# Optimization experiments

Hardware: AMD Instinct MI355X
Metric: run time of the kernel (lower is better)

## Reference

```python
import jax, jax.numpy as jnp
import numpy as np

V, E, H, B, T, O = 32000, 512, 1024, 128, 512, 1
PAD_IDX = 0


def setup_inputs() -> dict:
    key = jax.random.key(0)
    ks = jax.random.split(key, 20)
    std = 1.0 / np.sqrt(H)
    u = lambda k, shape: jax.random.uniform(k, shape, jnp.float32, -std, std)
    inp = {
        "x": jax.random.randint(ks[0], (B, T), 0, V),
        "lengths": jax.random.randint(ks[1], (B,), 1, T + 1),
        "emb": jax.random.normal(ks[2], (V, E), jnp.float32),
        "W_ii": u(ks[3], (H, E)), "W_hi": u(ks[4], (H, H)), "b_i": u(ks[5], (H,)),
        "W_if": u(ks[6], (H, E)), "W_hf": u(ks[7], (H, H)), "b_f": u(ks[8], (H,)),
        "W_ig": u(ks[9], (H, E)), "W_hg": u(ks[10], (H, H)), "b_g": u(ks[11], (H,)),
        "W_io": u(ks[12], (H, E)), "W_ho": u(ks[13], (H, H)), "b_o": u(ks[14], (H,)),
        "fc_w": u(ks[15], (O, H)), "fc_b": u(ks[16], (O,)),
    }
    return inp


def reference(x, lengths, emb, W_ii, W_hi, b_i, W_if, W_hf, b_f,
              W_ig, W_hg, b_g, W_io, W_ho, b_o, fc_w, fc_b):
    # padding_idx row is frozen at zero (matches nn.Embedding(padding_idx=...))
    emb = emb.at[PAD_IDX].set(0.0)
    xe = emb[x]  # [B, T, E]

    # stack the 4 gate projections (same math, one GEMM): gate order i, f, g, o
    Wi = jnp.concatenate([W_ii, W_if, W_ig, W_io], axis=0)  # [4H, E]
    Wh = jnp.concatenate([W_hi, W_hf, W_hg, W_ho], axis=0)  # [4H, H]
    b = jnp.concatenate([b_i, b_f, b_g, b_o], axis=0)       # [4H]

    # precompute all input contributions in one big GEMM: [B, T, 4H]
    xp = jnp.einsum('bte,ge->btg', xe, Wi) + b
    xp_t = jnp.transpose(xp, (1, 0, 2))  # [T, B, 4H]

    h0 = jnp.zeros((B, H), jnp.float32)
    c0 = jnp.zeros((B, H), jnp.float32)
    out0 = jnp.zeros((B, H), jnp.float32)
    ts = jnp.arange(T)

    def step(carry, inputs):
        h, c, out = carry
        xpt, t = inputs
        z = xpt + h @ Wh.T  # [B, 4H]
        i_t = jax.nn.sigmoid(z[:, 0 * H:1 * H])
        f_t = jax.nn.sigmoid(z[:, 1 * H:2 * H])
        g_t = jnp.tanh(z[:, 2 * H:3 * H])
        o_t = jax.nn.sigmoid(z[:, 3 * H:4 * H])
        c = f_t * c + i_t * g_t
        h = o_t * jnp.tanh(c)
        mask = (lengths == t + 1)[:, None]  # [B, 1]
        out = jnp.where(mask, h, out)
        return (h, c, out), None

    (_, _, outputs), _ = jax.lax.scan(step, (h0, c0, out0), (xp_t, ts))
    return outputs @ fc_w.T + fc_b  # [B, O]
```

## Files before the change

kernel.cpp:

```cpp
#include <hip/hip_runtime.h>
#include <math.h>

#define Bsz 128
#define Tsz 512
#define Esz 512
#define Hsz 1024
#define G4H 4096
#define Vsz 32000
#define NB  64
#define BH  (Bsz * Hsz)
#define XPS 68

typedef __attribute__((ext_vector_type(8))) short short8;
typedef __attribute__((ext_vector_type(4))) short short4v;
typedef __attribute__((ext_vector_type(8))) __bf16 bf16x8;
typedef __attribute__((ext_vector_type(4))) float f32x4;
typedef __attribute__((ext_vector_type(4))) unsigned int uint4v;

__device__ inline unsigned short f2bf(float f) {
    unsigned u = __float_as_uint(f);
    u += 0x7fffu + ((u >> 16) & 1u);
    return (unsigned short)(u >> 16);
}
__device__ inline float bf2f(unsigned short s) {
    return __uint_as_float(((unsigned)s) << 16);
}
__device__ inline f32x4 mfma16(short8 a, short8 b, f32x4 c) {
    return __builtin_amdgcn_mfma_f32_16x16x32_bf16(
        __builtin_bit_cast(bf16x8, a), __builtin_bit_cast(bf16x8, b), c, 0, 0, 0);
}

#define GLD16P(dst, p)  asm volatile("global_load_dwordx4 %0, %1, off"         : "=&v"(dst) : "v"(p))
#define GLD16C(dst, p)  asm volatile("global_load_dwordx4 %0, %1, off sc0 sc1" : "=&v"(dst) : "v"(p))

#define WAITVM(n)                                                          \
    do { asm volatile("s_waitcnt vmcnt(" #n ")" ::: "memory");             \
         __builtin_amdgcn_sched_barrier(0); } while (0)

__device__ inline unsigned ld_flag(const unsigned* p) {
    unsigned r;
    asm volatile("global_load_dword %0, %1, off sc0 sc1\n\ts_waitcnt vmcnt(0)"
                 : "=&v"(r) : "v"(p) : "memory");
    return r;
}
__device__ inline void st_flag(unsigned* p, unsigned v) {
    asm volatile("global_store_dword %0, %1, off sc0 sc1" :: "v"(p), "v"(v) : "memory");
}

__global__ void k_prep_emb(const float* __restrict__ emb, unsigned short* __restrict__ dst) {
    size_t i = (size_t)blockIdx.x * 256 + threadIdx.x;
    if (i < (size_t)Vsz * Esz) dst[i] = f2bf(i < Esz ? 0.f : emb[i]);
}

__global__ void k_prep_w(const float* __restrict__ wi, const float* __restrict__ wf,
                         const float* __restrict__ wg, const float* __restrict__ wo,
                         int ncols, unsigned short* __restrict__ dst) {
    size_t i = (size_t)blockIdx.x * 256 + threadIdx.x;
    size_t per = (size_t)Hsz * ncols;
    if (i < 4 * per) {
        int g = (int)(i / per);
        size_t rem = i - (size_t)g * per;
        const float* src = g == 0 ? wi : g == 1 ? wf : g == 2 ? wg : wo;
        dst[i] = f2bf(src[rem]);
    }
}

__global__ void k_prep_misc(const float* __restrict__ bi, const float* __restrict__ bff,
                            const float* __restrict__ bg, const float* __restrict__ bo,
                            float* __restrict__ b4, unsigned short* __restrict__ ghbuf,
                            float* __restrict__ cbuf, float* __restrict__ outh,
                            unsigned* __restrict__ flags) {
    int i = blockIdx.x * 256 + threadIdx.x;
    if (i < G4H) {
        const float* src = i < Hsz ? bi : i < 2 * Hsz ? bff : i < 3 * Hsz ? bg : bo;
        b4[i] = src[i & (Hsz - 1)];
    }
    if (i < 2 * BH) ghbuf[i] = 0;
    if (i < BH) { cbuf[i] = 0.f; outh[i] = 0.f; }
    if (i < NB * 32) flags[i] = 0u;
}

__global__ __launch_bounds__(256, 2) void xp_gemm(
    const unsigned short* __restrict__ emb16, const unsigned short* __restrict__ Wi16,
    const float* __restrict__ b4, const int* __restrict__ x,
    unsigned short* __restrict__ xp, int t_base)
{
    const int tp = blockIdx.x;
    const int n0 = blockIdx.y * 128;
    const int tid = threadIdx.x;
    const int w = tid >> 6, l = tid & 63;
    const int wm = w >> 1, wn = w & 1;
    const int lr = l & 15, lk = l >> 4;

    const unsigned short* arow[4];
    #pragma unroll
    for (int mt = 0; mt < 4; ++mt) {
        int b = wm * 64 + mt * 16 + lr;
        int xv = x[b * Tsz + t_base + tp];
        arow[mt] = emb16 + (size_t)xv * Esz + lk * 8;
    }
    const unsigned short* brow[4];
    #pragma unroll
    for (int nt = 0; nt < 4; ++nt) {
        int n = n0 + wn * 64 + nt * 16 + lr;
        brow[nt] = Wi16 + (size_t)n * Esz + lk * 8;
    }
    f32x4 acc[4][4] = {};
    #pragma unroll 2
    for (int k0 = 0; k0 < Esz; k0 += 32) {
        short8 av[4], bv[4];
        #pragma unroll
        for (int mt = 0; mt < 4; ++mt) av[mt] = *(const short8*)(arow[mt] + k0);
        #pragma unroll
        for (int nt = 0; nt < 4; ++nt) bv[nt] = *(const short8*)(brow[nt] + k0);
        #pragma unroll
        for (int mt = 0; mt < 4; ++mt)
            #pragma unroll
            for (int nt = 0; nt < 4; ++nt)
                acc[mt][nt] = mfma16(av[mt], bv[nt], acc[mt][nt]);
    }
    #pragma unroll
    for (int nt = 0; nt < 4; ++nt) {
        int n = n0 + wn * 64 + nt * 16 + lr;
        float bias = b4[n];
        int g = n >> 10, j = n & 1023;
        int bk = j >> 4, jj = j & 15;
        #pragma unroll
        for (int mt = 0; mt < 4; ++mt) {
            #pragma unroll
            for (int r = 0; r < 4; ++r) {
                int b = wm * 64 + mt * 16 + lk * 4 + r;
                xp[((size_t)tp * NB + bk) * (Bsz * 64) + b * 64 + jj * 4 + g] =
                    f2bf(acc[mt][nt][r] + bias);
            }
        }
    }
}

__global__ __launch_bounds__(512, 1) void lstm_steps(
    const unsigned short* __restrict__ Wh16,
    const unsigned short* __restrict__ xp,
    const int* __restrict__ lengths,
    unsigned short* __restrict__ ghbuf,
    float* __restrict__ cbuf,
    float* __restrict__ outh,
    unsigned* __restrict__ flags,
    int t0, int nsteps)
{
    __shared__ unsigned short Whs[64][1032];
    __shared__ unsigned short xps[Bsz * XPS];
    __shared__ unsigned short hls[Bsz * 16];
    const int tid = threadIdx.x;
    const int blk = blockIdx.x;
    const int j0 = blk * 16;

    for (int idx = tid; idx < 64 * 128; idx += 512) {
        int n = idx >> 7, gq = idx & 127;
        int grow = (n >> 4) * Hsz + j0 + (n & 15);
        *(short8*)&Whs[n][gq << 3] =
            *(const short8*)(Wh16 + (size_t)grow * Hsz + gq * 8);
    }

    const int w = tid >> 6, l = tid & 63, lr = l & 15, lk = l >> 4;

    int lenr[4];
    float creg[4];
    #pragma unroll
    for (int r = 0; r < 4; ++r) {
        int b = 16 * w + 4 * lk + r;
        lenr[r] = lengths[b];
        creg[r] = cbuf[(size_t)b * Hsz + j0 + lr];
    }

    {
        const short8* sp = (const short8*)(xp + (size_t)blk * (Bsz * 64));
        int xb = tid >> 2, xq = tid & 3;
        *(short8*)&xps[xb * XPS + xq * 16]     = sp[tid * 2];
        *(short8*)&xps[xb * XPS + xq * 16 + 8] = sp[tid * 2 + 1];
    }
    __syncthreads();

    const int hb_off = (lk >> 1) * 2048 + (lk & 1) * 8 + (16 * w + lr) * 16;

#define ISSUE_CHUNK(buf, kc_) do {                                         \
        GLD16C(buf[0], hb + (kc_) * 16384 + 0);                            \
        GLD16C(buf[1], hb + (kc_) * 16384 + 4096);                         \
        GLD16C(buf[2], hb + (kc_) * 16384 + 8192);                         \
        GLD16C(buf[3], hb + (kc_) * 16384 + 12288);                        \
    } while (0)

#define CONSUME(buf, kc_) do {                                             \
        _Pragma("unroll")                                                  \
        for (int ks_ = 0; ks_ < 4; ++ks_) {                                \
            short8 a_ = __builtin_bit_cast(short8, buf[ks_]);              \
            const int go_ = ((kc_) * 16 + ks_ * 4 + lk) << 3;              \
            _Pragma("unroll")                                              \
            for (int nt_ = 0; nt_ < 4; ++nt_) {                            \
                short8 bv_ = *(const short8*)&Whs[nt_ * 16 + lr][go_];     \
                acc[nt_] = mfma16(a_, bv_, acc[nt_]);                      \
            }                                                              \
        }                                                                  \
    } while (0)

    for (int s = 0; s < nsteps; ++s) {
        const int t = t0 + s;
        const unsigned short* hb = ghbuf + (size_t)(t & 1) * BH + hb_off;
        int sn = (s + 1 < nsteps) ? s + 1 : s;
        const unsigned short* xpn = xp + ((size_t)sn * NB + blk) * (Bsz * 64) + tid * 16;

        f32x4 acc[4] = {};
        uint4v A[4], Bb[4], xr0, xr1;
        ISSUE_CHUNK(A, 0);  ISSUE_CHUNK(Bb, 1);
        WAITVM(4);  CONSUME(A, 0);   ISSUE_CHUNK(A, 2);
        WAITVM(4);  CONSUME(Bb, 1);  ISSUE_CHUNK(Bb, 3);
        WAITVM(4);  CONSUME(A, 2);   ISSUE_CHUNK(A, 4);
        WAITVM(4);  CONSUME(Bb, 3);  ISSUE_CHUNK(Bb, 5);
        WAITVM(4);  CONSUME(A, 4);   ISSUE_CHUNK(A, 6);
        WAITVM(4);  CONSUME(Bb, 5);  ISSUE_CHUNK(Bb, 7);
        GLD16P(xr0, xpn); GLD16P(xr1, xpn + 8);
        WAITVM(6);  CONSUME(A, 6);
        WAITVM(2);  CONSUME(Bb, 7);

        #pragma unroll
        for (int r = 0; r < 4; ++r) {
            int b = 16 * w + 4 * lk + r;
            short4v xg4 = *(const short4v*)&xps[b * XPS + lr * 4];
            float zi = acc[0][r] + bf2f((unsigned short)xg4[0]);
            float zf = acc[1][r] + bf2f((unsigned short)xg4[1]);
            float zg = acc[2][r] + bf2f((unsigned short)xg4[2]);
            float zo = acc[3][r] + bf2f((unsigned short)xg4[3]);
            float it = 1.f / (1.f + __expf(-zi));
            float ft = 1.f / (1.f + __expf(-zf));
            float gt = tanhf(zg);
            float ot = 1.f / (1.f + __expf(-zo));
            float c = ft * creg[r] + it * gt;
            creg[r] = c;
            float h = ot * tanhf(c);
            if (lenr[r] == t + 1) outh[(size_t)b * Hsz + j0 + lr] = h;
            hls[b * 16 + lr] = f2bf(h);
        }
        __syncthreads();

        unsigned short* ghn = ghbuf + (size_t)((t + 1) & 1) * BH;
        if (tid < 256) {
            short8 hv8 = *(const short8*)&hls[tid * 8];
            unsigned short* hd = ghn + (size_t)blk * 2048 + tid * 8;
            asm volatile("global_store_dwordx4 %0, %1, off sc0 sc1"
                         :: "v"(hd), "v"(__builtin_bit_cast(uint4v, hv8)) : "memory");
        }

        WAITVM(0);
        {
            int xb = tid >> 2, xq = tid & 3;
            *(short8*)&xps[xb * XPS + xq * 16]     = __builtin_bit_cast(short8, xr0);
            *(short8*)&xps[xb * XPS + xq * 16 + 8] = __builtin_bit_cast(short8, xr1);
        }
        __syncthreads();

        if (tid == 0) st_flag(&flags[blk * 32], (unsigned)(t + 1));
        {
            const unsigned* fp = &flags[(tid & 63) * 32];
            while (ld_flag(fp) < (unsigned)(t + 1)) __builtin_amdgcn_s_sleep(1);
        }
        __syncthreads();
        __builtin_amdgcn_sched_barrier(0);
    }

    #pragma unroll
    for (int r = 0; r < 4; ++r) {
        int b = 16 * w + 4 * lk + r;
        cbuf[(size_t)b * Hsz + j0 + lr] = creg[r];
    }
#undef ISSUE_CHUNK
#undef CONSUME
}

__global__ __launch_bounds__(64) void k_fc(const float* __restrict__ outh,
                                           const float* __restrict__ fc_w,
                                           const float* __restrict__ fc_b,
                                           float* __restrict__ out) {
    int b = blockIdx.x, l = threadIdx.x;
    float s = 0.f;
    for (int k = l; k < Hsz; k += 64) s += outh[(size_t)b * Hsz + k] * fc_w[k];
    #pragma unroll
    for (int o = 32; o > 0; o >>= 1) s += __shfl_down(s, o);
    if (l == 0) out[b] = s + fc_b[0];
}

extern "C" void kernel_launch(void* const* d_in, const int* in_sizes, int n_in,
                              void* d_out, int out_size, void* d_ws, size_t ws_size,
                              hipStream_t stream) {
    const int* x       = (const int*)d_in[0];
    const int* lengths = (const int*)d_in[1];
    const float* emb   = (const float*)d_in[2];
    const float* W_ii  = (const float*)d_in[3];
    const float* W_hi  = (const float*)d_in[4];
    const float* b_i   = (const float*)d_in[5];
    const float* W_if  = (const float*)d_in[6];
    const float* W_hf  = (const float*)d_in[7];
    const float* b_f   = (const float*)d_in[8];
    const float* W_ig  = (const float*)d_in[9];
    const float* W_hg  = (const float*)d_in[10];
    const float* b_g   = (const float*)d_in[11];
    const float* W_io  = (const float*)d_in[12];
    const float* W_ho  = (const float*)d_in[13];
    const float* b_o   = (const float*)d_in[14];
    const float* fc_w  = (const float*)d_in[15];
    const float* fc_b  = (const float*)d_in[16];
    float* out = (float*)d_out;

    char* ws = (char*)d_ws;
    size_t off = 0;
    auto take = [&](size_t bytes) { size_t o = off; off += (bytes + 255) & ~(size_t)255; return o; };
    unsigned* flags       = (unsigned*)(ws + take((size_t)NB * 128));
    unsigned short* ghbuf = (unsigned short*)(ws + take((size_t)2 * BH * 2));
    float* cbuf           = (float*)(ws + take((size_t)BH * 4));
    float* outh           = (float*)(ws + take((size_t)BH * 4));
    float* b4             = (float*)(ws + take((size_t)G4H * 4));
    unsigned short* Wi16  = (unsigned short*)(ws + take((size_t)G4H * Esz * 2));
    unsigned short* Wh16  = (unsigned short*)(ws + take((size_t)G4H * Hsz * 2));
    unsigned short* emb16 = (unsigned short*)(ws + take((size_t)Vsz * Esz * 2));
    size_t fixed = off;

    int TC = 128;
    while (TC > 1 && fixed + (size_t)TC * Bsz * G4H * 2 > ws_size) TC >>= 1;
    unsigned short* xp = (unsigned short*)(ws + take((size_t)TC * Bsz * G4H * 2));

    k_prep_emb<<<(Vsz * Esz + 255) / 256, 256, 0, stream>>>(emb, emb16);
    k_prep_w<<<(4 * Hsz * Esz + 255) / 256, 256, 0, stream>>>(W_ii, W_if, W_ig, W_io, Esz, Wi16);
    k_prep_w<<<(4 * Hsz * Hsz + 255) / 256, 256, 0, stream>>>(W_hi, W_hf, W_hg, W_ho, Hsz, Wh16);
    k_prep_misc<<<(2 * BH + 255) / 256, 256, 0, stream>>>(b_i, b_f, b_g, b_o, b4, ghbuf, cbuf, outh, flags);

    for (int c = 0; c < Tsz / TC; ++c) {
        dim3 g(TC, 32);
        xp_gemm<<<g, 256, 0, stream>>>(emb16, Wi16, b4, x, xp, c * TC);
        lstm_steps<<<NB, 512, 0, stream>>>(Wh16, xp, lengths, ghbuf, cbuf, outh, flags, c * TC, TC);
    }
    k_fc<<<Bsz, 64, 0, stream>>>(outh, fc_w, fc_b, out);
}
```

Baseline: 4.809 ms.

## Switch recurrent step to 32x32x16 MFMA with 4 waves per block

Rewrites the persistent LSTM step kernel so each block uses 256 threads (4 waves) instead of 512. Each wave now computes a 32-batch by 64-gate tile with 32x32x16 bf16 MFMAs in place of 16x16x32 ones. The h loads are deepened to four chunks of eight 16-byte loads in flight, and a lane shuffle realigns the gate outputs before the elementwise update. The aim is fewer MFMA issues and fewer LDS reads of the weights per step. In exchange each wave does twice the per-lane elementwise work, uses more registers, and the block has fewer waves to hide the latency of the per-step grid barrier.

```diff
diff --git a/kernel.cpp b/kernel.cpp
--- a/kernel.cpp
+++ b/kernel.cpp
@@ -14,6 +14,7 @@
 typedef __attribute__((ext_vector_type(8))) short short8;
 typedef __attribute__((ext_vector_type(4))) short short4v;
 typedef __attribute__((ext_vector_type(8))) __bf16 bf16x8;
+typedef __attribute__((ext_vector_type(16))) float f32x16;
 typedef __attribute__((ext_vector_type(4))) float f32x4;
 typedef __attribute__((ext_vector_type(4))) unsigned int uint4v;
 
@@ -27,6 +28,10 @@
 }
 __device__ inline f32x4 mfma16(short8 a, short8 b, f32x4 c) {
     return __builtin_amdgcn_mfma_f32_16x16x32_bf16(
+        __builtin_bit_cast(bf16x8, a), __builtin_bit_cast(bf16x8, b), c, 0, 0, 0);
+}
+__device__ inline f32x16 mfma32(short8 a, short8 b, f32x16 c) {
+    return __builtin_amdgcn_mfma_f32_32x32x16_bf16(
         __builtin_bit_cast(bf16x8, a), __builtin_bit_cast(bf16x8, b), c, 0, 0, 0);
 }
 
@@ -137,7 +142,7 @@
     }
 }
 
-__global__ __launch_bounds__(512, 1) void lstm_steps(
+__global__ __launch_bounds__(256, 1) void lstm_steps(
     const unsigned short* __restrict__ Wh16,
     const unsigned short* __restrict__ xp,
     const int* __restrict__ lengths,
@@ -154,51 +159,62 @@
     const int blk = blockIdx.x;
     const int j0 = blk * 16;
 
-    for (int idx = tid; idx < 64 * 128; idx += 512) {
+    for (int idx = tid; idx < 64 * 128; idx += 256) {
         int n = idx >> 7, gq = idx & 127;
         int grow = (n >> 4) * Hsz + j0 + (n & 15);
         *(short8*)&Whs[n][gq << 3] =
             *(const short8*)(Wh16 + (size_t)grow * Hsz + gq * 8);
     }
 
-    const int w = tid >> 6, l = tid & 63, lr = l & 15, lk = l >> 4;
-
-    int lenr[4];
-    float creg[4];
-    #pragma unroll
-    for (int r = 0; r < 4; ++r) {
-        int b = 16 * w + 4 * lk + r;
-        lenr[r] = lengths[b];
-        creg[r] = cbuf[(size_t)b * Hsz + j0 + lr];
+    const int w = tid >> 6, l = tid & 63;
+    const int c31 = l & 31, jj = l & 15;
+    const int hi = (l >> 5) & 1;
+    const int hib = (l >> 4) & 1;
+    const bool lo = (hib == 0);
+
+    int lenr[8];
+    float creg[8];
+    #pragma unroll
+    for (int q = 0; q < 8; ++q) {
+        int row = (q & 3) + ((q >> 2) << 3) + (hi << 2) + (hib << 4);
+        int b = 32 * w + row;
+        lenr[q] = lengths[b];
+        creg[q] = cbuf[(size_t)b * Hsz + j0 + jj];
     }
 
     {
-        const short8* sp = (const short8*)(xp + (size_t)blk * (Bsz * 64));
-        int xb = tid >> 2, xq = tid & 3;
-        *(short8*)&xps[xb * XPS + xq * 16]     = sp[tid * 2];
-        *(short8*)&xps[xb * XPS + xq * 16 + 8] = sp[tid * 2 + 1];
+        const unsigned short* sp = xp + (size_t)blk * (Bsz * 64) + tid * 32;
+        int xb = tid >> 1, xq = tid & 1;
+        unsigned short* d = &xps[xb * XPS + xq * 32];
+        #pragma unroll
+        for (int u = 0; u < 4; ++u)
+            *(short8*)(d + u * 8) = *(const short8*)(sp + u * 8);
     }
     __syncthreads();
 
-    const int hb_off = (lk >> 1) * 2048 + (lk & 1) * 8 + (16 * w + lr) * 16;
+    const int hb_off = (32 * w + c31) * 16 + hi * 8;
+    const int bko = hi * 8;
 
 #define ISSUE_CHUNK(buf, kc_) do {                                         \
-        GLD16C(buf[0], hb + (kc_) * 16384 + 0);                            \
-        GLD16C(buf[1], hb + (kc_) * 16384 + 4096);                         \
-        GLD16C(buf[2], hb + (kc_) * 16384 + 8192);                         \
-        GLD16C(buf[3], hb + (kc_) * 16384 + 12288);                        \
+        GLD16C(buf[0], hb + (kc_) * 16384 + 0 * 2048);                     \
+        GLD16C(buf[1], hb + (kc_) * 16384 + 1 * 2048);                     \
+        GLD16C(buf[2], hb + (kc_) * 16384 + 2 * 2048);                     \
+        GLD16C(buf[3], hb + (kc_) * 16384 + 3 * 2048);                     \
+        GLD16C(buf[4], hb + (kc_) * 16384 + 4 * 2048);                     \
+        GLD16C(buf[5], hb + (kc_) * 16384 + 5 * 2048);                     \
+        GLD16C(buf[6], hb + (kc_) * 16384 + 6 * 2048);                     \
+        GLD16C(buf[7], hb + (kc_) * 16384 + 7 * 2048);                     \
     } while (0)
 
 #define CONSUME(buf, kc_) do {                                             \
         _Pragma("unroll")                                                  \
-        for (int ks_ = 0; ks_ < 4; ++ks_) {                                \
+        for (int ks_ = 0; ks_ < 8; ++ks_) {                                \
             short8 a_ = __builtin_bit_cast(short8, buf[ks_]);              \
-            const int go_ = ((kc_) * 16 + ks_ * 4 + lk) << 3;              \
-            _Pragma("unroll")                                              \
-            for (int nt_ = 0; nt_ < 4; ++nt_) {                            \
-                short8 bv_ = *(const short8*)&Whs[nt_ * 16 + lr][go_];     \
-                acc[nt_] = mfma16(a_, bv_, acc[nt_]);                      \
-            }                                                              \
+            const int ko_ = ((kc_) * 8 + ks_) * 16 + bko;                  \
+            short8 b0_ = *(const short8*)&Whs[c31][ko_];                   \
+            short8 b1_ = *(const short8*)&Whs[32 + c31][ko_];              \
+            acc0 = mfma32(a_, b0_, acc0);                                  \
+            acc1 = mfma32(a_, b1_, acc1);                                  \
         }                                                                  \
     } while (0)
 
@@ -206,43 +222,53 @@
         const int t = t0 + s;
         const unsigned short* hb = ghbuf + (size_t)(t & 1) * BH + hb_off;
         int sn = (s + 1 < nsteps) ? s + 1 : s;
-        const unsigned short* xpn = xp + ((size_t)sn * NB + blk) * (Bsz * 64) + tid * 16;
-
-        f32x4 acc[4] = {};
-        uint4v A[4], Bb[4], xr0, xr1;
-        ISSUE_CHUNK(A, 0);  ISSUE_CHUNK(Bb, 1);
-        WAITVM(4);  CONSUME(A, 0);   ISSUE_CHUNK(A, 2);
-        WAITVM(4);  CONSUME(Bb, 1);  ISSUE_CHUNK(Bb, 3);
-        WAITVM(4);  CONSUME(A, 2);   ISSUE_CHUNK(A, 4);
-        WAITVM(4);  CONSUME(Bb, 3);  ISSUE_CHUNK(Bb, 5);
-        WAITVM(4);  CONSUME(A, 4);   ISSUE_CHUNK(A, 6);
-        WAITVM(4);  CONSUME(Bb, 5);  ISSUE_CHUNK(Bb, 7);
+        const unsigned short* xpn = xp + ((size_t)sn * NB + blk) * (Bsz * 64) + tid * 32;
+
+        f32x16 acc0 = {}, acc1 = {};
+        uint4v P[8], Q[8], R[8], S[8], xr0, xr1, xr2, xr3;
+        ISSUE_CHUNK(P, 0); ISSUE_CHUNK(Q, 1); ISSUE_CHUNK(R, 2); ISSUE_CHUNK(S, 3);
+        WAITVM(24); CONSUME(P, 0); ISSUE_CHUNK(P, 4);
+        WAITVM(24); CONSUME(Q, 1); ISSUE_CHUNK(Q, 5);
+        WAITVM(24); CONSUME(R, 2); ISSUE_CHUNK(R, 6);
+        WAITVM(24); CONSUME(S, 3); ISSUE_CHUNK(S, 7);
+        WAITVM(24); CONSUME(P, 4);
         GLD16P(xr0, xpn); GLD16P(xr1, xpn + 8);
-        WAITVM(6);  CONSUME(A, 6);
-        WAITVM(2);  CONSUME(Bb, 7);
-
-        #pragma unroll
-        for (int r = 0; r < 4; ++r) {
-            int b = 16 * w + 4 * lk + r;
-            short4v xg4 = *(const short4v*)&xps[b * XPS + lr * 4];
-            float zi = acc[0][r] + bf2f((unsigned short)xg4[0]);
-            float zf = acc[1][r] + bf2f((unsigned short)xg4[1]);
-            float zg = acc[2][r] + bf2f((unsigned short)xg4[2]);
-            float zo = acc[3][r] + bf2f((unsigned short)xg4[3]);
+        GLD16P(xr2, xpn + 16); GLD16P(xr3, xpn + 24);
+        WAITVM(20); CONSUME(Q, 5);
+        WAITVM(12); CONSUME(R, 6);
+        WAITVM(4);  CONSUME(S, 7);
+
+        #pragma unroll
+        for (int q = 0; q < 8; ++q) {
+            float r0a = __shfl_xor(acc0[q], 16);
+            float r0b = __shfl_xor(acc0[q + 8], 16);
+            float r1a = __shfl_xor(acc1[q], 16);
+            float r1b = __shfl_xor(acc1[q + 8], 16);
+            float zi = lo ? acc0[q]     : r0b;
+            float zf = lo ? r0a         : acc0[q + 8];
+            float zg = lo ? acc1[q]     : r1b;
+            float zo = lo ? r1a         : acc1[q + 8];
+            int row = (q & 3) + ((q >> 2) << 3) + (hi << 2) + (hib << 4);
+            int b = 32 * w + row;
+            short4v xg4 = *(const short4v*)&xps[b * XPS + jj * 4];
+            zi += bf2f((unsigned short)xg4[0]);
+            zf += bf2f((unsigned short)xg4[1]);
+            zg += bf2f((unsigned short)xg4[2]);
+            zo += bf2f((unsigned short)xg4[3]);
             float it = 1.f / (1.f + __expf(-zi));
             float ft = 1.f / (1.f + __expf(-zf));
             float gt = tanhf(zg);
             float ot = 1.f / (1.f + __expf(-zo));
-            float c = ft * creg[r] + it * gt;
-            creg[r] = c;
+            float c = ft * creg[q] + it * gt;
+            creg[q] = c;
             float h = ot * tanhf(c);
-            if (lenr[r] == t + 1) outh[(size_t)b * Hsz + j0 + lr] = h;
-            hls[b * 16 + lr] = f2bf(h);
+            if (lenr[q] == t + 1) outh[(size_t)b * Hsz + j0 + jj] = h;
+            hls[b * 16 + jj] = f2bf(h);
         }
         __syncthreads();
 
         unsigned short* ghn = ghbuf + (size_t)((t + 1) & 1) * BH;
-        if (tid < 256) {
+        {
             short8 hv8 = *(const short8*)&hls[tid * 8];
             unsigned short* hd = ghn + (size_t)blk * 2048 + tid * 8;
             asm volatile("global_store_dwordx4 %0, %1, off sc0 sc1"
@@ -251,9 +277,12 @@
 
         WAITVM(0);
         {
-            int xb = tid >> 2, xq = tid & 3;
-            *(short8*)&xps[xb * XPS + xq * 16]     = __builtin_bit_cast(short8, xr0);
-            *(short8*)&xps[xb * XPS + xq * 16 + 8] = __builtin_bit_cast(short8, xr1);
+            int xb = tid >> 1, xq = tid & 1;
+            unsigned short* d = &xps[xb * XPS + xq * 32];
+            *(short8*)(d + 0)  = __builtin_bit_cast(short8, xr0);
+            *(short8*)(d + 8)  = __builtin_bit_cast(short8, xr1);
+            *(short8*)(d + 16) = __builtin_bit_cast(short8, xr2);
+            *(short8*)(d + 24) = __builtin_bit_cast(short8, xr3);
         }
         __syncthreads();
 
@@ -267,9 +296,10 @@
     }
 
     #pragma unroll
-    for (int r = 0; r < 4; ++r) {
-        int b = 16 * w + 4 * lk + r;
-        cbuf[(size_t)b * Hsz + j0 + lr] = creg[r];
+    for (int q = 0; q < 8; ++q) {
+        int row = (q & 3) + ((q >> 2) << 3) + (hi << 2) + (hib << 4);
+        int b = 32 * w + row;
+        cbuf[(size_t)b * Hsz + j0 + jj] = creg[q];
     }
 #undef ISSUE_CHUNK
 #undef CONSUME
@@ -334,7 +364,7 @@
     for (int c = 0; c < Tsz / TC; ++c) {
         dim3 g(TC, 32);
         xp_gemm<<<g, 256, 0, stream>>>(emb16, Wi16, b4, x, xp, c * TC);
-        lstm_steps<<<NB, 512, 0, stream>>>(Wh16, xp, lengths, ghbuf, cbuf, outh, flags, c * TC, TC);
+        lstm_steps<<<NB, 256, 0, stream>>>(Wh16, xp, lengths, ghbuf, cbuf, outh, flags, c * TC, TC);
     }
     k_fc<<<Bsz, 64, 0, stream>>>(outh, fc_w, fc_b, out);
 }
```

Result: slower. 5.787 ms (+20.3%).

## Replicate hidden state per XCD so recurrent loads hit local L2

Applied to the files above, without the earlier changes.

Each lstm_steps block finds its XCD id and a rank inside that XCD through an atomic counter. After every step the blocks on each XCD copy the full h vector from the MALL-coherent buffer into an XCD-private copy, and the next step reads h with L2-cached loads (sc0) instead of system-coherent ones. The aim is to cut the latency of the 128x1024 h reads in the recurrent GEMM. In exchange it adds a second grid-wide flag barrier, an extra copy phase per step, and a registration handshake at kernel start.

```diff
diff --git a/kernel.cpp b/kernel.cpp
--- a/kernel.cpp
+++ b/kernel.cpp
@@ -31,7 +31,9 @@
 }
 
 #define GLD16P(dst, p)  asm volatile("global_load_dwordx4 %0, %1, off"         : "=&v"(dst) : "v"(p))
-#define GLD16C(dst, p)  asm volatile("global_load_dwordx4 %0, %1, off sc0 sc1" : "=&v"(dst) : "v"(p))
+#define GLD16L2(dst, p) asm volatile("global_load_dwordx4 %0, %1, off sc0"     : "=&v"(dst) : "v"(p))
+#define GLD16M(dst, p)  asm volatile("global_load_dwordx4 %0, %1, off sc0 sc1" : "=&v"(dst) : "v"(p))
+#define ST16L2(p, v)    asm volatile("global_store_dwordx4 %0, %1, off sc0" :: "v"(p), "v"(v) : "memory")
 
 #define WAITVM(n)                                                          \
     do { asm volatile("s_waitcnt vmcnt(" #n ")" ::: "memory");             \
@@ -45,6 +47,12 @@
 }
 __device__ inline void st_flag(unsigned* p, unsigned v) {
     asm volatile("global_store_dword %0, %1, off sc0 sc1" :: "v"(p), "v"(v) : "memory");
+}
+__device__ inline unsigned atadd_mall(unsigned* p, unsigned v) {
+    unsigned old;
+    asm volatile("global_atomic_add %0, %1, %2, off sc0 sc1\n\ts_waitcnt vmcnt(0)"
+                 : "=&v"(old) : "v"(p), "v"(v) : "memory");
+    return old;
 }
 
 __global__ void k_prep_emb(const float* __restrict__ emb, unsigned short* __restrict__ dst) {
@@ -68,16 +76,20 @@
 __global__ void k_prep_misc(const float* __restrict__ bi, const float* __restrict__ bff,
                             const float* __restrict__ bg, const float* __restrict__ bo,
                             float* __restrict__ b4, unsigned short* __restrict__ ghbuf,
+                            unsigned short* __restrict__ xcopy,
                             float* __restrict__ cbuf, float* __restrict__ outh,
-                            unsigned* __restrict__ flags) {
-    int i = blockIdx.x * 256 + threadIdx.x;
+                            unsigned* __restrict__ flags, unsigned* __restrict__ flags2,
+                            unsigned* __restrict__ regflags, unsigned* __restrict__ xcdcnt) {
+    size_t i = (size_t)blockIdx.x * 256 + threadIdx.x;
     if (i < G4H) {
         const float* src = i < Hsz ? bi : i < 2 * Hsz ? bff : i < 3 * Hsz ? bg : bo;
         b4[i] = src[i & (Hsz - 1)];
     }
-    if (i < 2 * BH) ghbuf[i] = 0;
-    if (i < BH) { cbuf[i] = 0.f; outh[i] = 0.f; }
-    if (i < NB * 32) flags[i] = 0u;
+    if (i < 2 * (size_t)BH) ghbuf[i] = 0;
+    if (i < 16 * (size_t)BH) xcopy[i] = 0;
+    if (i < (size_t)BH) { cbuf[i] = 0.f; outh[i] = 0.f; }
+    if (i < NB * 32) { flags[i] = 0u; flags2[i] = 0u; regflags[i] = 0u; }
+    if (i < 128) xcdcnt[i] = 0u;
 }
 
 __global__ __launch_bounds__(256, 2) void xp_gemm(
@@ -142,14 +154,19 @@
     const unsigned short* __restrict__ xp,
     const int* __restrict__ lengths,
     unsigned short* __restrict__ ghbuf,
+    unsigned short* __restrict__ xcopy,
     float* __restrict__ cbuf,
     float* __restrict__ outh,
     unsigned* __restrict__ flags,
-    int t0, int nsteps)
+    unsigned* __restrict__ flags2,
+    unsigned* __restrict__ regflags,
+    unsigned* __restrict__ xcdcnt,
+    int launch_c, int t0, int nsteps)
 {
     __shared__ unsigned short Whs[64][1032];
     __shared__ unsigned short xps[Bsz * XPS];
     __shared__ unsigned short hls[Bsz * 16];
+    __shared__ int shx[3];
     const int tid = threadIdx.x;
     const int blk = blockIdx.x;
     const int j0 = blk * 16;
@@ -172,6 +189,24 @@
         creg[r] = cbuf[(size_t)b * Hsz + j0 + lr];
     }
 
+    if (tid == 0) {
+        unsigned xg;
+        asm volatile("s_getreg_b32 %0, hwreg(HW_REG_XCC_ID)" : "=s"(xg));
+        xg &= 7u;
+        unsigned rk = atadd_mall(&xcdcnt[launch_c * 8 + xg], 1u);
+        shx[0] = (int)xg;
+        shx[1] = (int)rk;
+        st_flag(&regflags[blk * 32], (unsigned)(launch_c + 1));
+    }
+    {
+        const unsigned* fp = &regflags[(tid & 63) * 32];
+        while (ld_flag(fp) < (unsigned)(launch_c + 1)) __builtin_amdgcn_s_sleep(1);
+    }
+    __syncthreads();
+    if (tid == 0) shx[2] = (int)ld_flag(&xcdcnt[launch_c * 8 + shx[0]]);
+    __syncthreads();
+    const int myx = shx[0], rank = shx[1], n_x = shx[2];
+
     {
         const short8* sp = (const short8*)(xp + (size_t)blk * (Bsz * 64));
         int xb = tid >> 2, xq = tid & 3;
@@ -183,10 +218,10 @@
     const int hb_off = (lk >> 1) * 2048 + (lk & 1) * 8 + (16 * w + lr) * 16;
 
 #define ISSUE_CHUNK(buf, kc_) do {                                         \
-        GLD16C(buf[0], hb + (kc_) * 16384 + 0);                            \
-        GLD16C(buf[1], hb + (kc_) * 16384 + 4096);                         \
-        GLD16C(buf[2], hb + (kc_) * 16384 + 8192);                         \
-        GLD16C(buf[3], hb + (kc_) * 16384 + 12288);                        \
+        GLD16L2(buf[0], hb + (kc_) * 16384 + 0);                           \
+        GLD16L2(buf[1], hb + (kc_) * 16384 + 4096);                        \
+        GLD16L2(buf[2], hb + (kc_) * 16384 + 8192);                        \
+        GLD16L2(buf[3], hb + (kc_) * 16384 + 12288);                       \
     } while (0)
 
 #define CONSUME(buf, kc_) do {                                             \
@@ -204,7 +239,7 @@
 
     for (int s = 0; s < nsteps; ++s) {
         const int t = t0 + s;
-        const unsigned short* hb = ghbuf + (size_t)(t & 1) * BH + hb_off;
+        const unsigned short* hb = xcopy + ((size_t)myx * 2 + (t & 1)) * BH + hb_off;
         int sn = (s + 1 < nsteps) ? s + 1 : s;
         const unsigned short* xpn = xp + ((size_t)sn * NB + blk) * (Bsz * 64) + tid * 16;
 
@@ -260,6 +295,32 @@
         if (tid == 0) st_flag(&flags[blk * 32], (unsigned)(t + 1));
         {
             const unsigned* fp = &flags[(tid & 63) * 32];
+            while (ld_flag(fp) < (unsigned)(t + 1)) __builtin_amdgcn_s_sleep(1);
+        }
+        __syncthreads();
+
+        {
+            unsigned short* xdst = xcopy + ((size_t)myx * 2 + ((t + 1) & 1)) * BH;
+            for (int p0 = rank; p0 < 32; p0 += n_x * 4) {
+                int p1 = p0 + n_x, p2 = p1 + n_x, p3 = p2 + n_x;
+                uint4v v0, v1, v2, v3;
+                GLD16M(v0, ghn + (size_t)p0 * 4096 + tid * 8);
+                if (p1 < 32) GLD16M(v1, ghn + (size_t)p1 * 4096 + tid * 8);
+                if (p2 < 32) GLD16M(v2, ghn + (size_t)p2 * 4096 + tid * 8);
+                if (p3 < 32) GLD16M(v3, ghn + (size_t)p3 * 4096 + tid * 8);
+                WAITVM(0);
+                ST16L2(xdst + (size_t)p0 * 4096 + tid * 8, v0);
+                if (p1 < 32) ST16L2(xdst + (size_t)p1 * 4096 + tid * 8, v1);
+                if (p2 < 32) ST16L2(xdst + (size_t)p2 * 4096 + tid * 8, v2);
+                if (p3 < 32) ST16L2(xdst + (size_t)p3 * 4096 + tid * 8, v3);
+            }
+            WAITVM(0);
+        }
+        __syncthreads();
+
+        if (tid == 0) st_flag(&flags2[blk * 32], (unsigned)(t + 1));
+        {
+            const unsigned* fp = &flags2[(tid & 63) * 32];
             while (ld_flag(fp) < (unsigned)(t + 1)) __builtin_amdgcn_s_sleep(1);
         }
         __syncthreads();
@@ -313,7 +374,11 @@
     size_t off = 0;
     auto take = [&](size_t bytes) { size_t o = off; off += (bytes + 255) & ~(size_t)255; return o; };
     unsigned* flags       = (unsigned*)(ws + take((size_t)NB * 128));
+    unsigned* flags2      = (unsigned*)(ws + take((size_t)NB * 128));
+    unsigned* regflags    = (unsigned*)(ws + take((size_t)NB * 128));
+    unsigned* xcdcnt      = (unsigned*)(ws + take(512));
     unsigned short* ghbuf = (unsigned short*)(ws + take((size_t)2 * BH * 2));
+    unsigned short* xcopy = (unsigned short*)(ws + take((size_t)16 * BH * 2));
     float* cbuf           = (float*)(ws + take((size_t)BH * 4));
     float* outh           = (float*)(ws + take((size_t)BH * 4));
     float* b4             = (float*)(ws + take((size_t)G4H * 4));
@@ -329,12 +394,15 @@
     k_prep_emb<<<(Vsz * Esz + 255) / 256, 256, 0, stream>>>(emb, emb16);
     k_prep_w<<<(4 * Hsz * Esz + 255) / 256, 256, 0, stream>>>(W_ii, W_if, W_ig, W_io, Esz, Wi16);
     k_prep_w<<<(4 * Hsz * Hsz + 255) / 256, 256, 0, stream>>>(W_hi, W_hf, W_hg, W_ho, Hsz, Wh16);
-    k_prep_misc<<<(2 * BH + 255) / 256, 256, 0, stream>>>(b_i, b_f, b_g, b_o, b4, ghbuf, cbuf, outh, flags);
+    k_prep_misc<<<(16 * BH + 255) / 256, 256, 0, stream>>>(
+        b_i, b_f, b_g, b_o, b4, ghbuf, xcopy, cbuf, outh, flags, flags2, regflags, xcdcnt);
 
     for (int c = 0; c < Tsz / TC; ++c) {
         dim3 g(TC, 32);
         xp_gemm<<<g, 256, 0, stream>>>(emb16, Wi16, b4, x, xp, c * TC);
-        lstm_steps<<<NB, 512, 0, stream>>>(Wh16, xp, lengths, ghbuf, cbuf, outh, flags, c * TC, TC);
+        lstm_steps<<<NB, 512, 0, stream>>>(Wh16, xp, lengths, ghbuf, xcopy, cbuf, outh,
+                                           flags, flags2, regflags, xcdcnt,
+                                           c, c * TC, TC);
     }
     k_fc<<<Bsz, 64, 0, stream>>>(outh, fc_w, fc_b, out);
 }
```

Result: slower. 5.754 ms (+19.6%).

## Overlap next chunk's input-projection GEMM with recurrent steps in one fused kernel

Applied to the files above, without the earlier changes.

The per-chunk input-projection GEMM becomes extra blocks (192 beyond the 64 recurrent blocks) of the LSTM step kernel. Those blocks compute the next chunk's gate inputs into a second buffer while the recurrent blocks consume the current one. Only the first chunk's GEMM still runs as a separate launch before the loop. The aim is to take the GEMM off the serial critical path. In exchange, the fused GEMM reads operands straight from global memory without LDS staging, and it may compete for memory bandwidth with the latency-bound recurrent blocks.

```diff
diff --git a/kernel.cpp b/kernel.cpp
--- a/kernel.cpp
+++ b/kernel.cpp
@@ -137,21 +137,85 @@
     }
 }
 
-__global__ __launch_bounds__(512, 1) void lstm_steps(
+__global__ __launch_bounds__(512, 1) void lstm_fused(
     const unsigned short* __restrict__ Wh16,
-    const unsigned short* __restrict__ xp,
+    const unsigned short* __restrict__ xpcur,
+    unsigned short* __restrict__ xpnext,
+    const unsigned short* __restrict__ emb16,
+    const unsigned short* __restrict__ Wi16,
+    const float* __restrict__ b4,
+    const int* __restrict__ x,
     const int* __restrict__ lengths,
     unsigned short* __restrict__ ghbuf,
     float* __restrict__ cbuf,
     float* __restrict__ outh,
     unsigned* __restrict__ flags,
-    int t0, int nsteps)
+    int t0, int nsteps, int gt_base, int do_gemm)
 {
     __shared__ unsigned short Whs[64][1032];
     __shared__ unsigned short xps[Bsz * XPS];
     __shared__ unsigned short hls[Bsz * 16];
     const int tid = threadIdx.x;
     const int blk = blockIdx.x;
+
+    if (blk >= NB) {
+        if (!do_gemm) return;
+        const int gb = blk - NB;
+        const int G = (int)gridDim.x - NB;
+        const int w = tid >> 6, l = tid & 63;
+        const int wm = w >> 2, wn = w & 3;
+        const int lr = l & 15, lk = l >> 4;
+        const int njobs = nsteps * 16;
+        for (int job = gb; job < njobs; job += G) {
+            int tp = job >> 4;
+            int n0 = (job & 15) * 256;
+            const unsigned short* arow[4];
+            #pragma unroll
+            for (int mt = 0; mt < 4; ++mt) {
+                int b = wm * 64 + mt * 16 + lr;
+                int xv = x[b * Tsz + gt_base + tp];
+                arow[mt] = emb16 + (size_t)xv * Esz + lk * 8;
+            }
+            const unsigned short* brow[4];
+            #pragma unroll
+            for (int nt = 0; nt < 4; ++nt) {
+                int n = n0 + wn * 64 + nt * 16 + lr;
+                brow[nt] = Wi16 + (size_t)n * Esz + lk * 8;
+            }
+            f32x4 acc[4][4] = {};
+            #pragma unroll 2
+            for (int k0 = 0; k0 < Esz; k0 += 32) {
+                short8 av[4], bv[4];
+                #pragma unroll
+                for (int mt = 0; mt < 4; ++mt) av[mt] = *(const short8*)(arow[mt] + k0);
+                #pragma unroll
+                for (int nt = 0; nt < 4; ++nt) bv[nt] = *(const short8*)(brow[nt] + k0);
+                #pragma unroll
+                for (int mt = 0; mt < 4; ++mt)
+                    #pragma unroll
+                    for (int nt = 0; nt < 4; ++nt)
+                        acc[mt][nt] = mfma16(av[mt], bv[nt], acc[mt][nt]);
+            }
+            #pragma unroll
+            for (int nt = 0; nt < 4; ++nt) {
+                int n = n0 + wn * 64 + nt * 16 + lr;
+                float bias = b4[n];
+                int g = n >> 10, j = n & 1023;
+                int bk = j >> 4, jj = j & 15;
+                #pragma unroll
+                for (int mt = 0; mt < 4; ++mt) {
+                    #pragma unroll
+                    for (int r = 0; r < 4; ++r) {
+                        int b = wm * 64 + mt * 16 + lk * 4 + r;
+                        xpnext[((size_t)tp * NB + bk) * (Bsz * 64) + b * 64 + jj * 4 + g] =
+                            f2bf(acc[mt][nt][r] + bias);
+                    }
+                }
+            }
+        }
+        return;
+    }
+
     const int j0 = blk * 16;
 
     for (int idx = tid; idx < 64 * 128; idx += 512) {
@@ -173,7 +237,7 @@
     }
 
     {
-        const short8* sp = (const short8*)(xp + (size_t)blk * (Bsz * 64));
+        const short8* sp = (const short8*)(xpcur + (size_t)blk * (Bsz * 64));
         int xb = tid >> 2, xq = tid & 3;
         *(short8*)&xps[xb * XPS + xq * 16]     = sp[tid * 2];
         *(short8*)&xps[xb * XPS + xq * 16 + 8] = sp[tid * 2 + 1];
@@ -206,7 +270,7 @@
         const int t = t0 + s;
         const unsigned short* hb = ghbuf + (size_t)(t & 1) * BH + hb_off;
         int sn = (s + 1 < nsteps) ? s + 1 : s;
-        const unsigned short* xpn = xp + ((size_t)sn * NB + blk) * (Bsz * 64) + tid * 16;
+        const unsigned short* xpn = xpcur + ((size_t)sn * NB + blk) * (Bsz * 64) + tid * 16;
 
         f32x4 acc[4] = {};
         uint4v A[4], Bb[4], xr0, xr1;
@@ -323,18 +387,26 @@
     size_t fixed = off;
 
     int TC = 128;
-    while (TC > 1 && fixed + (size_t)TC * Bsz * G4H * 2 > ws_size) TC >>= 1;
-    unsigned short* xp = (unsigned short*)(ws + take((size_t)TC * Bsz * G4H * 2));
+    while (TC > 1 && fixed + 2 * ((size_t)TC * Bsz * G4H * 2 + 256) > ws_size) TC >>= 1;
+    unsigned short* xp0 = (unsigned short*)(ws + take((size_t)TC * Bsz * G4H * 2));
+    unsigned short* xp1 = (unsigned short*)(ws + take((size_t)TC * Bsz * G4H * 2));
+    unsigned short* xpb[2] = {xp0, xp1};
 
     k_prep_emb<<<(Vsz * Esz + 255) / 256, 256, 0, stream>>>(emb, emb16);
     k_prep_w<<<(4 * Hsz * Esz + 255) / 256, 256, 0, stream>>>(W_ii, W_if, W_ig, W_io, Esz, Wi16);
     k_prep_w<<<(4 * Hsz * Hsz + 255) / 256, 256, 0, stream>>>(W_hi, W_hf, W_hg, W_ho, Hsz, Wh16);
     k_prep_misc<<<(2 * BH + 255) / 256, 256, 0, stream>>>(b_i, b_f, b_g, b_o, b4, ghbuf, cbuf, outh, flags);
 
-    for (int c = 0; c < Tsz / TC; ++c) {
+    const int nch = Tsz / TC;
+    {
         dim3 g(TC, 32);
-        xp_gemm<<<g, 256, 0, stream>>>(emb16, Wi16, b4, x, xp, c * TC);
-        lstm_steps<<<NB, 512, 0, stream>>>(Wh16, xp, lengths, ghbuf, cbuf, outh, flags, c * TC, TC);
+        xp_gemm<<<g, 256, 0, stream>>>(emb16, Wi16, b4, x, xp0, 0);
+    }
+    for (int c = 0; c < nch; ++c) {
+        lstm_fused<<<256, 512, 0, stream>>>(
+            Wh16, xpb[c & 1], xpb[(c + 1) & 1], emb16, Wi16, b4, x,
+            lengths, ghbuf, cbuf, outh, flags,
+            c * TC, TC, (c + 1) * TC, (c + 1 < nch) ? 1 : 0);
     }
     k_fc<<<Bsz, 64, 0, stream>>>(outh, fc_w, fc_b, out);
 }
```

New measurement: 3.906 ms. -18.8%, faster.
